# Performance work log

Measured on AMD Instinct MI355X. Metric: run time of the kernel, lower is better.

## Reference

```python
import jax, jax.numpy as jnp
import numpy as np

N, E = 50000, 800000
IN_C, HID, OUT_C = 128, 64, 40

def setup_inputs() -> dict:
    key = jax.random.key(0)
    ks = jax.random.split(key, 16)
    def w(k, shape, fan_in):
        return jax.random.normal(k, shape, dtype=jnp.float32) * (1.0 / np.sqrt(fan_in))
    x = jax.random.normal(ks[0], (N, IN_C), dtype=jnp.float32)
    edge_index = jax.random.randint(ks[1], (2, E), 0, N, dtype=jnp.int64)
    return {
        "x": x,
        "edge_index": edge_index,
        "W1": w(ks[2], (IN_C, HID), IN_C), "b1": jnp.zeros((HID,), jnp.float32),
        "W2": w(ks[3], (HID, HID), HID),   "b2": jnp.zeros((HID,), jnp.float32),
        "W3": w(ks[4], (HID, HID), HID),   "b3": jnp.zeros((HID,), jnp.float32),
        "g1": jnp.ones((HID,), jnp.float32), "be1": jnp.zeros((HID,), jnp.float32),
        "g2": jnp.ones((HID,), jnp.float32), "be2": jnp.zeros((HID,), jnp.float32),
        "M1": w(ks[5], (HID, HID), HID),   "mb1": jnp.zeros((HID,), jnp.float32),
        "M2": w(ks[6], (HID, OUT_C), HID), "mb2": jnp.zeros((OUT_C,), jnp.float32),
        "batch_size": N,
    }

def reference(x, edge_index, W1, b1, W2, b2, W3, b3, g1, be1, g2, be2, M1, mb1, M2, mb2, batch_size):
    src, dst = edge_index[0], edge_index[1]
    n = x.shape[0]
    # GCN symmetric norm with self-loops: deg over destination, +1 for self loop
    deg = jax.ops.segment_sum(jnp.ones(src.shape[0], x.dtype), dst, num_segments=n) + 1.0
    dinv = jax.lax.rsqrt(deg)  # deg >= 1 always
    enorm = (dinv[src] * dinv[dst])[:, None]  # [E,1]
    sloop = (dinv * dinv)[:, None]            # [N,1] self-loop norm

    def gcn_conv(h, W, b):
        hw = h @ W                                              # [N,H] transform first
        agg = jax.ops.segment_sum(enorm * hw[src], dst, num_segments=n)
        return agg + sloop * hw + b

    def layer_norm(h, g, be):
        mu = jnp.mean(h, axis=-1, keepdims=True)
        var = jnp.var(h, axis=-1, keepdims=True)
        return (h - mu) * jax.lax.rsqrt(var + 1e-5) * g + be

    h = jax.nn.relu(layer_norm(gcn_conv(x, W1, b1), g1, be1))
    h = jax.nn.relu(layer_norm(gcn_conv(h, W2, b2), g2, be2))
    h = gcn_conv(h, W3, b3)
    # MLP: Linear -> ReLU -> Linear
    h = jax.nn.relu(h @ M1 + mb1) @ M2 + mb2
    return jax.nn.softmax(h[:batch_size], axis=1)
```

## Files before the change

### kernel.cpp

```cpp
#include <hip/hip_runtime.h>
#include <hip/hip_fp16.h>
#include <math.h>

#define HID   64
#define OUTC  40
#define CAP   64

__global__ void zero_kernel(int4* __restrict__ p, int n4) {
    int i = blockIdx.x * blockDim.x + threadIdx.x;
    if (i < n4) p[i] = make_int4(0, 0, 0, 0);
}

__global__ void fill_kernel(const int* __restrict__ src, const int* __restrict__ dst,
                            int* __restrict__ cnt, unsigned short* __restrict__ recs,
                            int E, int N) {
    int g    = blockIdx.x & 7;
    int gblk = blockIdx.x >> 3;
    int nblk = gridDim.x >> 3;
    int slice = (N + 7) >> 3;
    int lo = g * slice;
    int hi = lo + slice; if (hi > N) hi = N;
    for (int e = gblk * blockDim.x + threadIdx.x; e < E; e += nblk * blockDim.x) {
        int d = dst[e];
        if (d >= lo && d < hi) {
            int pos = atomicAdd(&cnt[d], 1);
            if (pos < CAP) recs[(size_t)d * CAP + pos] = (unsigned short)src[e];
        }
    }
}

__global__ __launch_bounds__(256) void w3m1_kernel(const float* __restrict__ W3,
                                                   const float* __restrict__ M1,
                                                   const float* __restrict__ b3,
                                                   const float* __restrict__ mb1,
                                                   float* __restrict__ W3M1,
                                                   float* __restrict__ b31) {
    __shared__ float M1s[64][68];
    int tid = threadIdx.x;
    {
        int k = tid >> 4, c = (tid & 15) << 2;
        #pragma unroll
        for (int k0 = 0; k0 < 64; k0 += 16)
            *(float4*)&M1s[k0 + k][c] = *(const float4*)(M1 + ((size_t)(k0 + k) << 6) + c);
    }
    __syncthreads();
    int row = (blockIdx.x << 4) + (tid >> 4);
    int c4  = (tid & 15) << 2;
    float a0 = 0.f, a1 = 0.f, a2 = 0.f, a3 = 0.f;
    const float* wr = W3 + ((size_t)row << 6);
    #pragma unroll 4
    for (int j = 0; j < 64; j++) {
        float w = wr[j];
        float4 m = *(const float4*)&M1s[j][c4];
        a0 = fmaf(w, m.x, a0); a1 = fmaf(w, m.y, a1);
        a2 = fmaf(w, m.z, a2); a3 = fmaf(w, m.w, a3);
    }
    *(float4*)(W3M1 + ((size_t)row << 6) + c4) = make_float4(a0, a1, a2, a3);
    if (blockIdx.x == 0 && tid < 64) {
        float acc = mb1[tid];
        #pragma unroll 4
        for (int k = 0; k < 64; k++) acc = fmaf(b3[k], M1s[k][tid], acc);
        b31[tid] = acc;
    }
}

#define FMA16(acc, a, b) \
    acc[0][0] = fmaf(a.x, b.x, acc[0][0]); acc[0][1] = fmaf(a.x, b.y, acc[0][1]); \
    acc[0][2] = fmaf(a.x, b.z, acc[0][2]); acc[0][3] = fmaf(a.x, b.w, acc[0][3]); \
    acc[1][0] = fmaf(a.y, b.x, acc[1][0]); acc[1][1] = fmaf(a.y, b.y, acc[1][1]); \
    acc[1][2] = fmaf(a.y, b.z, acc[1][2]); acc[1][3] = fmaf(a.y, b.w, acc[1][3]); \
    acc[2][0] = fmaf(a.z, b.x, acc[2][0]); acc[2][1] = fmaf(a.z, b.y, acc[2][1]); \
    acc[2][2] = fmaf(a.z, b.z, acc[2][2]); acc[2][3] = fmaf(a.z, b.w, acc[2][3]); \
    acc[3][0] = fmaf(a.w, b.x, acc[3][0]); acc[3][1] = fmaf(a.w, b.y, acc[3][1]); \
    acc[3][2] = fmaf(a.w, b.z, acc[3][2]); acc[3][3] = fmaf(a.w, b.w, acc[3][3]);

template<int CIN, typename T>
__global__ __launch_bounds__(256) void xform_kernel(const T* __restrict__ X,
                                                    const float* __restrict__ W,
                                                    const int* __restrict__ cnt,
                                                    __half* __restrict__ out, int N) {
    __shared__ float Xs[CIN][68];
    __shared__ float Ws[CIN][68];
    int tid = threadIdx.x;
    int base = blockIdx.x << 6;
    int rows = N - base; if (rows > 64) rows = 64;

    {
        int k = tid >> 4, c = (tid & 15) << 2;
        #pragma unroll
        for (int k0 = 0; k0 < CIN; k0 += 16) {
            float4 wv = *(const float4*)(W + (size_t)((k0 + k) << 6) + c);
            *(float4*)&Ws[k0 + k][c] = wv;
        }
    }
    {
        int r = tid >> 2, q = (tid & 3) << 2;
        int rc = r < rows ? r : 0;
        const T* xp = X + (size_t)(base + rc) * CIN + q;
        #pragma unroll
        for (int k0 = 0; k0 < CIN; k0 += 16) {
            float4 xv;
            if constexpr (sizeof(T) == 4) {
                xv = *(const float4*)(xp + k0);
            } else {
                union { uint2 u; __half2 h[2]; } pk;
                pk.u = *(const uint2*)(xp + k0);
                float2 f01 = __half22float2(pk.h[0]);
                float2 f23 = __half22float2(pk.h[1]);
                xv = make_float4(f01.x, f01.y, f23.x, f23.y);
            }
            Xs[k0 + q + 0][r] = xv.x;
            Xs[k0 + q + 1][r] = xv.y;
            Xs[k0 + q + 2][r] = xv.z;
            Xs[k0 + q + 3][r] = xv.w;
        }
    }
    __syncthreads();

    int tx = tid & 15, ty = tid >> 4;
    float acc[4][4] = {};
    #pragma unroll 4
    for (int k = 0; k < CIN; k++) {
        float4 a = *(const float4*)&Xs[k][ty << 2];
        float4 b = *(const float4*)&Ws[k][tx << 2];
        FMA16(acc, a, b)
    }
    #pragma unroll
    for (int rr = 0; rr < 4; rr++) {
        int row = (ty << 2) + rr;
        if (row < rows) {
            float di = rsqrtf((float)cnt[base + row] + 1.0f);
            union { uint2 u; __half2 h[2]; } pk;
            pk.h[0] = __float22half2_rn(make_float2(acc[rr][0] * di, acc[rr][1] * di));
            pk.h[1] = __float22half2_rn(make_float2(acc[rr][2] * di, acc[rr][3] * di));
            *(uint2*)(out + ((size_t)(base + row) << 6) + (tx << 2)) = pk.u;
        }
    }
    if (blockIdx.x == gridDim.x - 1 && tid < 8) {
        uint4 z = make_uint4(0, 0, 0, 0);
        ((uint4*)(out + ((size_t)N << 6)))[tid] = z;
    }
}

template<bool LN, bool RELU>
__global__ void conv_kernel(const __half* __restrict__ hwh,
                            const unsigned short* __restrict__ recs,
                            const int* __restrict__ cnt,
                            const float* __restrict__ b, const float* __restrict__ g,
                            const float* __restrict__ be, __half* __restrict__ out, int N) {
    int lane = threadIdx.x & 63;
    int row  = (blockIdx.x << 2) + (threadIdx.x >> 6);
    if (row >= N) return;

    int cn = cnt[row];
    int c  = cn > CAP ? CAP : cn;
    int s_l = N;
    if (lane < c) s_l = recs[(size_t)row * CAP + lane];

    int g4 = lane >> 4, j = lane & 15;
    const uint2* hw8 = (const uint2*)hwh;
    float di = rsqrtf((float)cn + 1.0f);
    uint2 selfv = hw8[(size_t)row * 16 + j];

    float acc[4] = {0, 0, 0, 0};
    int kmax = (c + 7) & ~7;
    for (int k = 0; k < kmax; k += 8) {
        int s0 = __shfl(s_l, k + g4), s1 = __shfl(s_l, k + 4 + g4);
        uint2 v0 = hw8[(size_t)s0 * 16 + j];
        uint2 v1 = hw8[(size_t)s1 * 16 + j];
        const __half2* h0 = (const __half2*)&v0;
        const __half2* h1 = (const __half2*)&v1;
        #pragma unroll
        for (int t = 0; t < 2; t++) {
            float2 f0 = __half22float2(h0[t]);
            float2 f1 = __half22float2(h1[t]);
            acc[2*t]   += f0.x + f1.x;
            acc[2*t+1] += f0.y + f1.y;
        }
    }
    #pragma unroll
    for (int off = 16; off < 64; off <<= 1) {
        #pragma unroll
        for (int t = 0; t < 4; t++) acc[t] += __shfl_xor(acc[t], off);
    }

    int f0 = j << 2;
    const __half2* sp = (const __half2*)&selfv;
    float4 bb = *(const float4*)(b + f0);
    {
        float2 fa = __half22float2(sp[0]);
        float2 fb = __half22float2(sp[1]);
        acc[0] = fmaf(di, acc[0] + fa.x, bb.x);
        acc[1] = fmaf(di, acc[1] + fa.y, bb.y);
        acc[2] = fmaf(di, acc[2] + fb.x, bb.z);
        acc[3] = fmaf(di, acc[3] + fb.y, bb.w);
    }

    if (LN) {
        float s = (acc[0] + acc[1]) + (acc[2] + acc[3]);
        #pragma unroll
        for (int o = 1; o < 16; o <<= 1) s += __shfl_xor(s, o);
        float mu = s * (1.f / 64.f);
        float v = 0.f;
        #pragma unroll
        for (int t = 0; t < 4; t++) { acc[t] -= mu; v += acc[t] * acc[t]; }
        #pragma unroll
        for (int o = 1; o < 16; o <<= 1) v += __shfl_xor(v, o);
        float r = rsqrtf(v * (1.f / 64.f) + 1e-5f);
        float4 gg = *(const float4*)(g + f0);
        float4 eb = *(const float4*)(be + f0);
        acc[0] = fmaxf(fmaf(acc[0] * r, gg.x, eb.x), 0.f);
        acc[1] = fmaxf(fmaf(acc[1] * r, gg.y, eb.y), 0.f);
        acc[2] = fmaxf(fmaf(acc[2] * r, gg.z, eb.z), 0.f);
        acc[3] = fmaxf(fmaf(acc[3] * r, gg.w, eb.w), 0.f);
    } else if (RELU) {
        #pragma unroll
        for (int t = 0; t < 4; t++) acc[t] = fmaxf(acc[t], 0.f);
    }
    if (g4 == 0) {
        union { uint2 u; __half2 h[2]; } pk;
        pk.h[0] = __float22half2_rn(make_float2(acc[0], acc[1]));
        pk.h[1] = __float22half2_rn(make_float2(acc[2], acc[3]));
        *(uint2*)(out + (size_t)row * 64 + f0) = pk.u;
    }
}

__global__ __launch_bounds__(256) void mlp_kernel(const __half* __restrict__ h,
                           const float* __restrict__ M2, const float* __restrict__ mb2,
                           float* __restrict__ out, int N) {
    __shared__ float Hs [64][68];
    __shared__ float W2s[64][44];
    int tid = threadIdx.x;
    int base = blockIdx.x << 6;
    int rows = N - base; if (rows > 64) rows = 64;

    for (int i = tid; i < 64 * OUTC; i += 256)
        W2s[i / OUTC][i % OUTC] = M2[i];
    {
        int r = tid >> 2, q = (tid & 3) << 2;
        int rc = r < rows ? r : 0;
        const __half* xp = h + (((size_t)(base + rc)) << 6) + q;
        #pragma unroll
        for (int k0 = 0; k0 < 64; k0 += 16) {
            union { uint2 u; __half2 hh[2]; } pk;
            pk.u = *(const uint2*)(xp + k0);
            float2 f01 = __half22float2(pk.hh[0]);
            float2 f23 = __half22float2(pk.hh[1]);
            Hs[k0 + q + 0][r] = f01.x;
            Hs[k0 + q + 1][r] = f01.y;
            Hs[k0 + q + 2][r] = f23.x;
            Hs[k0 + q + 3][r] = f23.y;
        }
    }
    __syncthreads();

    int tx = tid & 15, ty = tid >> 4;
    int bx = (tx < 10) ? (tx << 2) : 0;
    float acc2[4][4] = {};
    #pragma unroll 4
    for (int k = 0; k < 64; k++) {
        float4 a = *(const float4*)&Hs[k][ty << 2];
        float4 b = *(const float4*)&W2s[k][bx];
        FMA16(acc2, a, b)
    }
    float4 b2v = *(const float4*)(mb2 + bx);

    #pragma unroll
    for (int rr = 0; rr < 4; rr++) {
        float v0 = acc2[rr][0] + b2v.x, v1 = acc2[rr][1] + b2v.y;
        float v2 = acc2[rr][2] + b2v.z, v3 = acc2[rr][3] + b2v.w;
        float m = fmaxf(fmaxf(v0, v1), fmaxf(v2, v3));
        if (tx >= 10) m = -1e30f;
        #pragma unroll
        for (int s = 1; s < 16; s <<= 1) m = fmaxf(m, __shfl_xor(m, s));
        float e0 = __expf(v0 - m), e1 = __expf(v1 - m);
        float e2 = __expf(v2 - m), e3 = __expf(v3 - m);
        float sum = (tx < 10) ? (e0 + e1) + (e2 + e3) : 0.f;
        #pragma unroll
        for (int s = 1; s < 16; s <<= 1) sum += __shfl_xor(sum, s);
        float inv = 1.f / sum;
        int row = (ty << 2) + rr;
        if (tx < 10 && row < rows)
            *(float4*)(out + (size_t)(base + row) * OUTC + bx) =
                make_float4(e0 * inv, e1 * inv, e2 * inv, e3 * inv);
    }
}

extern "C" void kernel_launch(void* const* d_in, const int* in_sizes, int n_in,
                              void* d_out, int out_size, void* d_ws, size_t ws_size,
                              hipStream_t stream) {
    const float* x   = (const float*)d_in[0];
    const int*   ei  = (const int*)  d_in[1];
    const float* W1  = (const float*)d_in[2];
    const float* b1  = (const float*)d_in[3];
    const float* W2  = (const float*)d_in[4];
    const float* b2  = (const float*)d_in[5];
    const float* W3  = (const float*)d_in[6];
    const float* b3  = (const float*)d_in[7];
    const float* g1  = (const float*)d_in[8];
    const float* be1 = (const float*)d_in[9];
    const float* g2  = (const float*)d_in[10];
    const float* be2 = (const float*)d_in[11];
    const float* M1  = (const float*)d_in[12];
    const float* mb1 = (const float*)d_in[13];
    const float* M2  = (const float*)d_in[14];
    const float* mb2 = (const float*)d_in[15];

    const int IN_C = 128;
    int N = in_sizes[0] / IN_C;
    int E = in_sizes[1] / 2;
    const int* src = ei;
    const int* dst = ei + E;

    char* ws = (char*)d_ws;
    size_t off = 0;
    auto carve = [&](size_t bytes) -> void* {
        void* p = ws + off;
        off = (off + bytes + 255) & ~(size_t)255;
        return p;
    };
    int*            cnt  = (int*)           carve(((size_t)N + 4) * sizeof(int));
    unsigned short* recs = (unsigned short*)carve((size_t)N * CAP * sizeof(unsigned short));
    __half*         HWh  = (__half*)        carve((size_t)(N + 1) * HID * sizeof(__half));
    __half*         H    = (__half*)        carve((size_t)(N + 1) * HID * sizeof(__half));
    __half*         H3   = (__half*)        carve((size_t)(N + 1) * HID * sizeof(__half));
    float*          W3M1 = (float*)         carve((size_t)HID * HID * sizeof(float));
    float*          b31  = (float*)         carve((size_t)HID * sizeof(float));

    int n4 = (N + 3) / 4;
    zero_kernel<<<(n4 + 255) / 256, 256, 0, stream>>>((int4*)cnt, n4);

    int rb = (N + 3) / 4;
    int tb = (N + 63) / 64;

    fill_kernel<<<2048, 256, 0, stream>>>(src, dst, cnt, recs, E, N);
    w3m1_kernel<<<4, 256, 0, stream>>>(W3, M1, b3, mb1, W3M1, b31);

    xform_kernel<128, float><<<tb, 256, 0, stream>>>(x, W1, cnt, HWh, N);
    conv_kernel<true, false><<<rb, 256, 0, stream>>>(HWh, recs, cnt, b1, g1, be1, H, N);
    xform_kernel<64, __half><<<tb, 256, 0, stream>>>(H, W2, cnt, HWh, N);
    conv_kernel<true, false><<<rb, 256, 0, stream>>>(HWh, recs, cnt, b2, g2, be2, H, N);
    xform_kernel<64, __half><<<tb, 256, 0, stream>>>(H, W3M1, cnt, HWh, N);
    conv_kernel<false, true><<<rb, 256, 0, stream>>>(HWh, recs, cnt, b31, nullptr, nullptr, H3, N);

    mlp_kernel<<<tb, 256, 0, stream>>>(H3, M2, mb2, (float*)d_out, N);
}
```

Baseline: 182.5 us.

## Merge zero and W3M1 setup kernels, unroll conv gather, widen fill grid

Folds the count-zeroing kernel and the W3·M1 precompute into one setup kernel, so there is one fewer launch. Unrolls the neighbor gather loop in the conv kernel to issue four row loads per iteration instead of two, which raises memory-level parallelism. Doubles the fill_kernel grid from 2048 to 4096 blocks. The launch saving is small, and the unroll may raise register pressure.

```diff
diff --git a/kernel.cpp b/kernel.cpp
--- a/kernel.cpp
+++ b/kernel.cpp
@@ -6,9 +6,45 @@
 #define OUTC  40
 #define CAP   64
 
-__global__ void zero_kernel(int4* __restrict__ p, int n4) {
-    int i = blockIdx.x * blockDim.x + threadIdx.x;
-    if (i < n4) p[i] = make_int4(0, 0, 0, 0);
+__global__ __launch_bounds__(256) void setup_kernel(const float* __restrict__ W3,
+                                                    const float* __restrict__ M1,
+                                                    const float* __restrict__ b3,
+                                                    const float* __restrict__ mb1,
+                                                    float* __restrict__ W3M1,
+                                                    float* __restrict__ b31,
+                                                    int4* __restrict__ cnt4, int n4) {
+    int tid = threadIdx.x;
+    if (blockIdx.x >= 4) {
+        int i = (blockIdx.x - 4) * blockDim.x + tid;
+        if (i < n4) cnt4[i] = make_int4(0, 0, 0, 0);
+        return;
+    }
+    __shared__ float M1s[64][68];
+    {
+        int k = tid >> 4, c = (tid & 15) << 2;
+        #pragma unroll
+        for (int k0 = 0; k0 < 64; k0 += 16)
+            *(float4*)&M1s[k0 + k][c] = *(const float4*)(M1 + ((size_t)(k0 + k) << 6) + c);
+    }
+    __syncthreads();
+    int row = (blockIdx.x << 4) + (tid >> 4);
+    int c4  = (tid & 15) << 2;
+    float a0 = 0.f, a1 = 0.f, a2 = 0.f, a3 = 0.f;
+    const float* wr = W3 + ((size_t)row << 6);
+    #pragma unroll 4
+    for (int j = 0; j < 64; j++) {
+        float w = wr[j];
+        float4 m = *(const float4*)&M1s[j][c4];
+        a0 = fmaf(w, m.x, a0); a1 = fmaf(w, m.y, a1);
+        a2 = fmaf(w, m.z, a2); a3 = fmaf(w, m.w, a3);
+    }
+    *(float4*)(W3M1 + ((size_t)row << 6) + c4) = make_float4(a0, a1, a2, a3);
+    if (blockIdx.x == 0 && tid < 64) {
+        float acc = mb1[tid];
+        #pragma unroll 4
+        for (int k = 0; k < 64; k++) acc = fmaf(b3[k], M1s[k][tid], acc);
+        b31[tid] = acc;
+    }
 }
 
 __global__ void fill_kernel(const int* __restrict__ src, const int* __restrict__ dst,
@@ -26,41 +62,6 @@
             int pos = atomicAdd(&cnt[d], 1);
             if (pos < CAP) recs[(size_t)d * CAP + pos] = (unsigned short)src[e];
         }
-    }
-}
-
-__global__ __launch_bounds__(256) void w3m1_kernel(const float* __restrict__ W3,
-                                                   const float* __restrict__ M1,
-                                                   const float* __restrict__ b3,
-                                                   const float* __restrict__ mb1,
-                                                   float* __restrict__ W3M1,
-                                                   float* __restrict__ b31) {
-    __shared__ float M1s[64][68];
-    int tid = threadIdx.x;
-    {
-        int k = tid >> 4, c = (tid & 15) << 2;
-        #pragma unroll
-        for (int k0 = 0; k0 < 64; k0 += 16)
-            *(float4*)&M1s[k0 + k][c] = *(const float4*)(M1 + ((size_t)(k0 + k) << 6) + c);
-    }
-    __syncthreads();
-    int row = (blockIdx.x << 4) + (tid >> 4);
-    int c4  = (tid & 15) << 2;
-    float a0 = 0.f, a1 = 0.f, a2 = 0.f, a3 = 0.f;
-    const float* wr = W3 + ((size_t)row << 6);
-    #pragma unroll 4
-    for (int j = 0; j < 64; j++) {
-        float w = wr[j];
-        float4 m = *(const float4*)&M1s[j][c4];
-        a0 = fmaf(w, m.x, a0); a1 = fmaf(w, m.y, a1);
-        a2 = fmaf(w, m.z, a2); a3 = fmaf(w, m.w, a3);
-    }
-    *(float4*)(W3M1 + ((size_t)row << 6) + c4) = make_float4(a0, a1, a2, a3);
-    if (blockIdx.x == 0 && tid < 64) {
-        float acc = mb1[tid];
-        #pragma unroll 4
-        for (int k = 0; k < 64; k++) acc = fmaf(b3[k], M1s[k][tid], acc);
-        b31[tid] = acc;
     }
 }
 
@@ -164,7 +165,29 @@
 
     float acc[4] = {0, 0, 0, 0};
     int kmax = (c + 7) & ~7;
-    for (int k = 0; k < kmax; k += 8) {
+    int k = 0;
+    for (; k + 16 <= kmax; k += 16) {
+        int s0 = __shfl(s_l, k + g4),      s1 = __shfl(s_l, k + 4 + g4);
+        int s2 = __shfl(s_l, k + 8 + g4),  s3 = __shfl(s_l, k + 12 + g4);
+        uint2 v0 = hw8[(size_t)s0 * 16 + j];
+        uint2 v1 = hw8[(size_t)s1 * 16 + j];
+        uint2 v2 = hw8[(size_t)s2 * 16 + j];
+        uint2 v3 = hw8[(size_t)s3 * 16 + j];
+        const __half2* h0 = (const __half2*)&v0;
+        const __half2* h1 = (const __half2*)&v1;
+        const __half2* h2 = (const __half2*)&v2;
+        const __half2* h3 = (const __half2*)&v3;
+        #pragma unroll
+        for (int t = 0; t < 2; t++) {
+            float2 f0 = __half22float2(h0[t]);
+            float2 f1 = __half22float2(h1[t]);
+            float2 f2 = __half22float2(h2[t]);
+            float2 f3 = __half22float2(h3[t]);
+            acc[2*t]   += (f0.x + f1.x) + (f2.x + f3.x);
+            acc[2*t+1] += (f0.y + f1.y) + (f2.y + f3.y);
+        }
+    }
+    if (k < kmax) {
         int s0 = __shfl(s_l, k + g4), s1 = __shfl(s_l, k + 4 + g4);
         uint2 v0 = hw8[(size_t)s0 * 16 + j];
         uint2 v1 = hw8[(size_t)s1 * 16 + j];
@@ -328,13 +351,12 @@
     float*          b31  = (float*)         carve((size_t)HID * sizeof(float));
 
     int n4 = (N + 3) / 4;
-    zero_kernel<<<(n4 + 255) / 256, 256, 0, stream>>>((int4*)cnt, n4);
-
     int rb = (N + 3) / 4;
     int tb = (N + 63) / 64;
 
-    fill_kernel<<<2048, 256, 0, stream>>>(src, dst, cnt, recs, E, N);
-    w3m1_kernel<<<4, 256, 0, stream>>>(W3, M1, b3, mb1, W3M1, b31);
+    setup_kernel<<<4 + (n4 + 255) / 256, 256, 0, stream>>>(W3, M1, b3, mb1, W3M1, b31,
+                                                           (int4*)cnt, n4);
+    fill_kernel<<<4096, 256, 0, stream>>>(src, dst, cnt, recs, E, N);
 
     xform_kernel<128, float><<<tb, 256, 0, stream>>>(x, W1, cnt, HWh, N);
     conv_kernel<true, false><<<rb, 256, 0, stream>>>(HWh, recs, cnt, b1, g1, be1, H, N);
```

Result: faster. 173.1 us (-5.2%).
